# Performance work log

Measured on AMD Instinct MI355X. Metric: run time of the kernel, lower is better.

The kernel has to match this reference:

```python
import jax, jax.numpy as jnp
import numpy as np

EMBED_DIM = 768
NUM_HEADS = 8
HEAD_DIM = EMBED_DIM // NUM_HEADS  # 96
SCALE = HEAD_DIM ** -0.5


def setup_inputs() -> dict:
    key = jax.random.key(0)
    k1, k2, k3 = jax.random.split(key, 3)
    x = jax.random.normal(k1, (2, 4096, EMBED_DIM), dtype=jnp.float32)
    # nn.Linear weights stored [out, in]; init scaled like kaiming-uniform-ish
    w_qkv = jax.random.normal(k2, (3 * EMBED_DIM, EMBED_DIM), dtype=jnp.float32) * (EMBED_DIM ** -0.5)
    w_proj = jax.random.normal(k3, (EMBED_DIM, EMBED_DIM), dtype=jnp.float32) * (EMBED_DIM ** -0.5)
    return {"x": x, "w_qkv": w_qkv, "w_proj": w_proj}


def reference(x, w_qkv, w_proj):
    B, N, C = x.shape
    H, D = NUM_HEADS, C // NUM_HEADS
    qkv = jnp.einsum('bnc,oc->bno', x, w_qkv)          # [B,N,3C]
    qkv = qkv.reshape(B, N, 3, H, D).transpose(2, 0, 3, 1, 4)  # [3,B,H,N,D]
    q, k, v = qkv[0], qkv[1], qkv[2]
    attn = jnp.einsum('bhnd,bhmd->bhnm', q, k) * SCALE  # [B,H,N,N]
    attn = jax.nn.softmax(attn, axis=-1)
    out = jnp.einsum('bhnm,bhmd->bhnd', attn, v)        # [B,H,N,D]
    out = out.transpose(0, 2, 1, 3).reshape(B, N, C)
    out = jnp.einsum('bnc,oc->bno', out, w_proj)        # proj (no bias)
    return out  # dropout p=0.0 -> identity
```

## Files before the change

### kernel.cpp

```cpp
#include <hip/hip_runtime.h>

typedef __bf16 bf16;
typedef __attribute__((ext_vector_type(8))) __bf16 bf16x8;
typedef __attribute__((ext_vector_type(2))) __bf16 bf16x2;
typedef __attribute__((ext_vector_type(4))) float f32x4;
typedef __attribute__((ext_vector_type(16))) float f32x16;
typedef __attribute__((ext_vector_type(8))) unsigned short ushort8;
typedef __attribute__((ext_vector_type(4))) unsigned short ushort4v;

__device__ __forceinline__ unsigned short f2bf(float f) {
    union { float f; unsigned int u; } v; v.f = f;
    unsigned int u = v.u;
    return (unsigned short)((u + 0x7fffu + ((u >> 16) & 1u)) >> 16);
}

#if __has_builtin(__builtin_amdgcn_cvt_pk_bf16_f32)
__device__ __forceinline__ unsigned int pk2bf(float a, float b) {
    union { bf16x2 v; unsigned int u; } c;
    c.v = __builtin_amdgcn_cvt_pk_bf16_f32(a, b);
    return c.u;
}
#else
__device__ __forceinline__ unsigned int pk2bf(float a, float b) {
    return (unsigned int)f2bf(a) | ((unsigned int)f2bf(b) << 16);
}
#endif

__device__ __forceinline__ f32x4 mfma16(bf16x8 a, bf16x8 b, f32x4 c) {
    return __builtin_amdgcn_mfma_f32_16x16x32_bf16(a, b, c, 0, 0, 0);
}
__device__ __forceinline__ f32x16 mfma32(bf16x8 a, bf16x8 b, f32x16 c) {
    return __builtin_amdgcn_mfma_f32_32x32x16_bf16(a, b, c, 0, 0, 0);
}

#if __has_builtin(__builtin_amdgcn_global_load_lds)
__device__ __forceinline__ void gload16(const unsigned short* g, unsigned short* l) {
    typedef const unsigned int __attribute__((address_space(1)))* gp_t;
    typedef unsigned int __attribute__((address_space(3)))* lp_t;
    __builtin_amdgcn_global_load_lds((gp_t)(const void*)g, (lp_t)(void*)l, 16, 0, 0);
}
#define GLL_LANE 1
#else
#define GLL_LANE 0
#endif

__global__ void cvt3_f32_bf16(const float* __restrict__ x, const float* __restrict__ wq,
                              const float* __restrict__ wp,
                              unsigned short* __restrict__ xb, unsigned short* __restrict__ wqb,
                              unsigned short* __restrict__ wpb) {
    int i = blockIdx.x * 256 + threadIdx.x;
    const float* in; unsigned short* out; int base;
    if (i < 1572864)      { in = x;  out = xb;  base = i; }
    else if (i < 2015232) { in = wq; out = wqb; base = i - 1572864; }
    else if (i < 2162688) { in = wp; out = wpb; base = i - 2015232; }
    else return;
    float4 f = reinterpret_cast<const float4*>(in)[base];
    union { ushort4v v; unsigned int u[2]; } o;
    o.u[0] = pk2bf(f.x, f.y);
    o.u[1] = pk2bf(f.z, f.w);
    reinterpret_cast<ushort4v*>(out)[base] = o.v;
}

__device__ __forceinline__ int kperm(int k5) {
    return (k5 & 3) | (((k5 >> 3) & 1) << 2) | (((k5 >> 4) & 1) << 3) | (((k5 >> 2) & 1) << 4);
}
__device__ __forceinline__ int kperm_inv(int p5) {
    return (p5 & 3) | (((p5 >> 4) & 1) << 2) | (((p5 >> 2) & 1) << 3) | (((p5 >> 3) & 1) << 4);
}

__global__ __launch_bounds__(256) void qkv_gemm(const unsigned short* __restrict__ A,
                                                const unsigned short* __restrict__ W,
                                                unsigned short* __restrict__ Qf,
                                                unsigned short* __restrict__ Kf,
                                                unsigned short* __restrict__ Vf) {
    __shared__ __align__(16) char smem[34816];
    unsigned short* As = (unsigned short*)smem;
    unsigned short* Bs = (unsigned short*)(smem + 8192);
    unsigned short* T  = (unsigned short*)smem;
    const int t = threadIdx.x;
    const int w = t >> 6, l = t & 63;
    const int wm = (w >> 1) * 64, wn = (w & 1) * 64;
    const int lr = l & 15, lq = l >> 4;
    const int m0 = blockIdx.y * 128, n0 = blockIdx.x * 128;
    f32x4 acc[4][4] = {};
    for (int k0 = 0; k0 < 768; k0 += 32) {
        __syncthreads();
#pragma unroll
        for (int i = 0; i < 2; ++i) {
            int v = t + i * 256;
            int r = v >> 2, c8 = (v & 3) * 8;
#if GLL_LANE
            gload16(&A[(m0 + r) * 768 + k0 + c8], &As[(w * 64 + i * 256) * 8]);
            gload16(&W[(n0 + r) * 768 + k0 + c8], &Bs[(w * 64 + i * 256) * 8]);
#else
            *reinterpret_cast<ushort8*>(&As[r * 32 + c8]) =
                *reinterpret_cast<const ushort8*>(&A[(m0 + r) * 768 + k0 + c8]);
            *reinterpret_cast<ushort8*>(&Bs[r * 32 + c8]) =
                *reinterpret_cast<const ushort8*>(&W[(n0 + r) * 768 + k0 + c8]);
#endif
        }
        __syncthreads();
        bf16x8 af[4], bfr[4];
#pragma unroll
        for (int mt = 0; mt < 4; ++mt)
            af[mt] = *reinterpret_cast<const bf16x8*>(&As[(wm + mt * 16 + lr) * 32 + lq * 8]);
#pragma unroll
        for (int nt = 0; nt < 4; ++nt)
            bfr[nt] = *reinterpret_cast<const bf16x8*>(&Bs[(wn + nt * 16 + lr) * 32 + lq * 8]);
#pragma unroll
        for (int mt = 0; mt < 4; ++mt)
#pragma unroll
            for (int nt = 0; nt < 4; ++nt)
                acc[mt][nt] = mfma16(af[mt], bfr[nt], acc[mt][nt]);
    }
    const int tsel = n0 / 768;
    __syncthreads();
    if (tsel < 2) {
#pragma unroll
        for (int nt = 0; nt < 4; ++nt)
#pragma unroll
            for (int mt = 0; mt < 4; ++mt)
#pragma unroll
                for (int r = 0; r < 4; ++r) {
                    int row = wm + mt * 16 + lq * 4 + r;
                    int col = wn + nt * 16 + lr;
                    float val = acc[mt][nt][r];
                    if (tsel == 0) val *= 0.14724444f;
                    T[row * 136 + col] = f2bf(val);
                }
    } else {
#pragma unroll
        for (int nt = 0; nt < 4; ++nt)
#pragma unroll
            for (int mt = 0; mt < 4; ++mt)
#pragma unroll
                for (int r = 0; r < 4; ++r) {
                    int row = wm + mt * 16 + lq * 4 + r;
                    int col = wn + nt * 16 + lr;
                    T[col * 136 + row] = f2bf(acc[mt][nt][r]);
                }
    }
    __syncthreads();
    if (tsel < 2) {
#pragma unroll
        for (int i = 0; i < 8; ++i) {
            int idx = t + i * 256;
            int pos31 = idx & 31;
            int rest = idx >> 5;
            int c8 = rest & 15, qg = rest >> 4;
            int l31 = (tsel == 1) ? kperm_inv(pos31) : pos31;
            int gncol = n0 + c8 * 8;
            int rem = gncol - tsel * 768;
            int head = rem / 96, d = rem - head * 96;
            int kq = d >> 4, h2 = (d >> 3) & 1;
            int gm = m0 + qg * 32 + l31;
            int b = gm >> 12, nn = gm & 4095;
            int bh = b * 8 + head;
            long chunk = (long)(bh * 128 + (nn >> 5)) * 6 + kq;
            ushort8 v8 = *reinterpret_cast<const ushort8*>(&T[(qg * 32 + l31) * 136 + c8 * 8]);
            unsigned short* dst = (tsel == 0) ? Qf : Kf;
            *reinterpret_cast<ushort8*>(&dst[(chunk << 9) + ((h2 * 32 + pos31) << 3)]) = v8;
        }
    } else {
#pragma unroll
        for (int i = 0; i < 8; ++i) {
            int idx = t + i * 256;
            int dl = idx & 31;
            int rr = idx >> 5;
            int r8 = rr & 15, cmb = rr >> 4;
            int col = cmb * 32 + dl;
            int gncol = n0 + col;
            int rem = gncol - 1536;
            int head = rem / 96, d = rem - head * 96;
            int dn = d >> 5;
            int keybase = m0 + r8 * 8;
            int b = keybase >> 12, nn = keybase & 4095;
            int kg = nn >> 5, f = (nn >> 4) & 1, hv = (nn >> 3) & 1;
            int bh = b * 8 + head;
            long chunk = (long)(bh * 128 + kg) * 6 + dn * 2 + f;
            ushort8 v8 = *reinterpret_cast<const ushort8*>(&T[col * 136 + r8 * 8]);
            *reinterpret_cast<ushort8*>(&Vf[(chunk << 9) + ((hv * 32 + dl) << 3)]) = v8;
        }
    }
}

__global__ __launch_bounds__(256, 2) void attn_kernel(const unsigned short* __restrict__ Qf,
                                                      const unsigned short* __restrict__ Kf,
                                                      const unsigned short* __restrict__ Vf,
                                                      unsigned short* __restrict__ Og) {
    __shared__ __align__(16) float red[4608];
    const int t = threadIdx.x;
    const int w = t >> 6, l = t & 63;
    const int wr = w >> 1, wk = w & 1;
    const int l31 = l & 31, h = l >> 5;
    const int b0 = blockIdx.x;
    const int kk = b0 >> 3;
    const int bh = (b0 & 7) * 2 + (kk >> 5);
    const int q0 = (kk & 31) * 128;
    const int voff = l << 3;

    bf16x8 aq[2][6];
#pragma unroll
    for (int qn = 0; qn < 2; ++qn) {
        long qb = ((long)((bh * 128 + (q0 >> 5) + wr * 2 + qn) * 6)) << 9;
#pragma unroll
        for (int kq = 0; kq < 6; ++kq)
            aq[qn][kq] = *reinterpret_cast<const bf16x8*>(&Qf[qb + (kq << 9) + voff]);
    }

    f32x16 acc[2][3] = {};
    float lsum0 = 0.f, lsum1 = 0.f;

    for (int it = 0; it < 64; ++it) {
        const int kt = wk * 64 + it;
        const long kbase = ((long)((bh * 128 + kt) * 6)) << 9;
        f32x16 s[2] = {};
#pragma unroll
        for (int kq = 0; kq < 6; ++kq) {
            bf16x8 bk = *reinterpret_cast<const bf16x8*>(&Kf[kbase + (kq << 9) + voff]);
            s[0] = mfma32(bk, aq[0][kq], s[0]);
            s[1] = mfma32(bk, aq[1][kq], s[1]);
        }
        union PF { unsigned int u[4]; bf16x8 v8; } p[2][2];
#pragma unroll
        for (int qn = 0; qn < 2; ++qn) {
            float e[16];
#pragma unroll
            for (int r = 0; r < 16; ++r) e[r] = __builtin_amdgcn_exp2f(s[qn][r]);
            float s0 = (e[0] + e[1]) + (e[2] + e[3]);
            float s1 = (e[4] + e[5]) + (e[6] + e[7]);
            float s2 = (e[8] + e[9]) + (e[10] + e[11]);
            float s3 = (e[12] + e[13]) + (e[14] + e[15]);
            if (qn == 0) lsum0 += (s0 + s1) + (s2 + s3);
            else         lsum1 += (s0 + s1) + (s2 + s3);
#pragma unroll
            for (int f = 0; f < 2; ++f) {
                p[qn][f].u[0] = pk2bf(e[4 * f + 0], e[4 * f + 1]);
                p[qn][f].u[1] = pk2bf(e[4 * f + 2], e[4 * f + 3]);
                p[qn][f].u[2] = pk2bf(e[8 + 4 * f + 0], e[8 + 4 * f + 1]);
                p[qn][f].u[3] = pk2bf(e[8 + 4 * f + 2], e[8 + 4 * f + 3]);
            }
        }
#pragma unroll
        for (int dn = 0; dn < 3; ++dn) {
#pragma unroll
            for (int f = 0; f < 2; ++f) {
                bf16x8 vb = *reinterpret_cast<const bf16x8*>(
                    &Vf[kbase + ((dn * 2 + f) << 9) + voff]);
                acc[0][dn] = mfma32(p[0][f].v8, vb, acc[0][dn]);
                acc[1][dn] = mfma32(p[1][f].v8, vb, acc[1][dn]);
            }
        }
    }

    const int rbase = (wr * 64 + l) * 36;
#pragma unroll
    for (int ps = 0; ps < 3; ++ps) {
        __syncthreads();
        if (wk == 1) {
#pragma unroll
            for (int c = 0; c < 2; ++c) {
                int c2 = ps * 2 + c, qn = c2 / 3, dn = c2 % 3;
#pragma unroll
                for (int u = 0; u < 4; ++u) {
                    f32x4 tmp;
#pragma unroll
                    for (int j = 0; j < 4; ++j) tmp[j] = acc[qn][dn][u * 4 + j];
                    *reinterpret_cast<f32x4*>(&red[rbase + c * 16 + u * 4]) = tmp;
                }
            }
        }
        __syncthreads();
        if (wk == 0) {
#pragma unroll
            for (int c = 0; c < 2; ++c) {
                int c2 = ps * 2 + c, qn = c2 / 3, dn = c2 % 3;
#pragma unroll
                for (int u = 0; u < 4; ++u) {
                    f32x4 tmp = *reinterpret_cast<const f32x4*>(&red[rbase + c * 16 + u * 4]);
#pragma unroll
                    for (int j = 0; j < 4; ++j) acc[qn][dn][u * 4 + j] += tmp[j];
                }
            }
        }
    }

    lsum0 += __shfl_xor(lsum0, 32);
    lsum1 += __shfl_xor(lsum1, 32);
    __syncthreads();
    if (wk == 1 && h == 0) {
        red[(wr * 2 + 0) * 32 + l31] = lsum0;
        red[(wr * 2 + 1) * 32 + l31] = lsum1;
    }
    __syncthreads();
    if (wk == 0 && h == 0) {
        red[128 + (wr * 2 + 0) * 32 + l31] = 1.f / (lsum0 + red[(wr * 2 + 0) * 32 + l31]);
        red[128 + (wr * 2 + 1) * 32 + l31] = 1.f / (lsum1 + red[(wr * 2 + 1) * 32 + l31]);
    }
    __syncthreads();
    if (wk == 0) {
        const int b = bh >> 3, head = bh & 7;
#pragma unroll
        for (int qn = 0; qn < 2; ++qn) {
#pragma unroll
            for (int reg = 0; reg < 16; ++reg) {
                int qloc = (reg & 3) + 8 * (reg >> 2) + 4 * h;
                int n = q0 + wr * 64 + qn * 32 + qloc;
                float inv = red[128 + (wr * 2 + qn) * 32 + qloc];
                int rowoff = (b * 4096 + n) * 768 + head * 96;
#pragma unroll
                for (int dn = 0; dn < 3; ++dn)
                    Og[rowoff + dn * 32 + l31] = f2bf(acc[qn][dn][reg] * inv);
            }
        }
    }
}

__global__ __launch_bounds__(256) void proj_gemm(const unsigned short* __restrict__ A,
                                                 const unsigned short* __restrict__ W,
                                                 float* __restrict__ out) {
    __shared__ __align__(16) unsigned short As[128 * 32];
    __shared__ __align__(16) unsigned short Bs[128 * 32];
    const int t = threadIdx.x;
    const int w = t >> 6, l = t & 63;
    const int wm = (w >> 1) * 64, wn = (w & 1) * 64;
    const int lr = l & 15, lq = l >> 4;
    const int m0 = blockIdx.y * 128, n0 = blockIdx.x * 128;
    f32x4 acc[4][4] = {};
    for (int k0 = 0; k0 < 768; k0 += 32) {
        __syncthreads();
#pragma unroll
        for (int i = 0; i < 2; ++i) {
            int v = t + i * 256;
            int r = v >> 2, c8 = (v & 3) * 8;
#if GLL_LANE
            gload16(&A[(m0 + r) * 768 + k0 + c8], &As[(w * 64 + i * 256) * 8]);
            gload16(&W[(n0 + r) * 768 + k0 + c8], &Bs[(w * 64 + i * 256) * 8]);
#else
            *reinterpret_cast<ushort8*>(&As[r * 32 + c8]) =
                *reinterpret_cast<const ushort8*>(&A[(m0 + r) * 768 + k0 + c8]);
            *reinterpret_cast<ushort8*>(&Bs[r * 32 + c8]) =
                *reinterpret_cast<const ushort8*>(&W[(n0 + r) * 768 + k0 + c8]);
#endif
        }
        __syncthreads();
        bf16x8 af[4], bfr[4];
#pragma unroll
        for (int mt = 0; mt < 4; ++mt)
            af[mt] = *reinterpret_cast<const bf16x8*>(&As[(wm + mt * 16 + lr) * 32 + lq * 8]);
#pragma unroll
        for (int nt = 0; nt < 4; ++nt)
            bfr[nt] = *reinterpret_cast<const bf16x8*>(&Bs[(wn + nt * 16 + lr) * 32 + lq * 8]);
#pragma unroll
        for (int mt = 0; mt < 4; ++mt)
#pragma unroll
            for (int nt = 0; nt < 4; ++nt)
                acc[mt][nt] = mfma16(af[mt], bfr[nt], acc[mt][nt]);
    }
#pragma unroll
    for (int nt = 0; nt < 4; ++nt) {
        int gn = n0 + wn + nt * 16 + lr;
#pragma unroll
        for (int mt = 0; mt < 4; ++mt) {
#pragma unroll
            for (int r = 0; r < 4; ++r) {
                int gm = m0 + wm + mt * 16 + lq * 4 + r;
                out[gm * 768 + gn] = acc[mt][nt][r];
            }
        }
    }
}

extern "C" void kernel_launch(void* const* d_in, const int* in_sizes, int n_in,
                              void* d_out, int out_size, void* d_ws, size_t ws_size,
                              hipStream_t stream) {
    const float* x     = (const float*)d_in[0];
    const float* wqkv  = (const float*)d_in[1];
    const float* wproj = (const float*)d_in[2];
    float* out = (float*)d_out;
    char* ws = (char*)d_ws;
    unsigned short* xb     = (unsigned short*)(ws);
    unsigned short* wqkvb  = (unsigned short*)(ws + 12582912);
    unsigned short* wprojb = (unsigned short*)(ws + 16121856);
    unsigned short* Qf     = (unsigned short*)(ws + 17301504);
    unsigned short* Kf     = (unsigned short*)(ws + 29884416);
    unsigned short* Vf     = (unsigned short*)(ws + 42467328);
    unsigned short* attnb  = xb;

    cvt3_f32_bf16<<<8448, 256, 0, stream>>>(x, wqkv, wproj, xb, wqkvb, wprojb);
    qkv_gemm<<<dim3(18, 64), 256, 0, stream>>>(xb, wqkvb, Qf, Kf, Vf);
    attn_kernel<<<512, 256, 0, stream>>>(Qf, Kf, Vf, attnb);
    proj_gemm<<<dim3(6, 64), 256, 0, stream>>>(attnb, wprojb, out);
}
```

Measured before the change: 270.3 us.

## Halve attention query tile per block to double grid and occupancy

The attention kernel now gives each block 64 query rows instead of 128, so each wave handles one 32-row query slab rather than two. Register and shared-memory use per block roughly halve, launch bounds rise to 4 blocks per CU, and the grid doubles to 1024 blocks, aiming for better latency hiding and CU fill on a 256-CU part. In exchange, each K/V fragment loaded from global memory now feeds only one query slab, doubling K/V traffic per unit of work and lowering MFMA reuse per load.

```diff
diff --git a/kernel.cpp b/kernel.cpp
--- a/kernel.cpp
+++ b/kernel.cpp
@@ -184,62 +184,51 @@
     }
 }
 
-__global__ __launch_bounds__(256, 2) void attn_kernel(const unsigned short* __restrict__ Qf,
+__global__ __launch_bounds__(256, 4) void attn_kernel(const unsigned short* __restrict__ Qf,
                                                       const unsigned short* __restrict__ Kf,
                                                       const unsigned short* __restrict__ Vf,
                                                       unsigned short* __restrict__ Og) {
-    __shared__ __align__(16) float red[4608];
+    __shared__ __align__(16) float red[2560];
     const int t = threadIdx.x;
     const int w = t >> 6, l = t & 63;
     const int wr = w >> 1, wk = w & 1;
     const int l31 = l & 31, h = l >> 5;
     const int b0 = blockIdx.x;
     const int kk = b0 >> 3;
-    const int bh = (b0 & 7) * 2 + (kk >> 5);
-    const int q0 = (kk & 31) * 128;
+    const int bh = (b0 & 7) * 2 + (kk >> 6);
+    const int q0 = (kk & 63) * 64;
     const int voff = l << 3;
 
-    bf16x8 aq[2][6];
-#pragma unroll
-    for (int qn = 0; qn < 2; ++qn) {
-        long qb = ((long)((bh * 128 + (q0 >> 5) + wr * 2 + qn) * 6)) << 9;
+    bf16x8 aq[6];
+    {
+        long qb = ((long)((bh * 128 + (q0 >> 5) + wr) * 6)) << 9;
 #pragma unroll
         for (int kq = 0; kq < 6; ++kq)
-            aq[qn][kq] = *reinterpret_cast<const bf16x8*>(&Qf[qb + (kq << 9) + voff]);
-    }
-
-    f32x16 acc[2][3] = {};
-    float lsum0 = 0.f, lsum1 = 0.f;
+            aq[kq] = *reinterpret_cast<const bf16x8*>(&Qf[qb + (kq << 9) + voff]);
+    }
+
+    f32x16 acc[3] = {};
+    float lsum = 0.f;
 
     for (int it = 0; it < 64; ++it) {
         const int kt = wk * 64 + it;
         const long kbase = ((long)((bh * 128 + kt) * 6)) << 9;
-        f32x16 s[2] = {};
+        f32x16 s = {};
 #pragma unroll
         for (int kq = 0; kq < 6; ++kq) {
             bf16x8 bk = *reinterpret_cast<const bf16x8*>(&Kf[kbase + (kq << 9) + voff]);
-            s[0] = mfma32(bk, aq[0][kq], s[0]);
-            s[1] = mfma32(bk, aq[1][kq], s[1]);
-        }
-        union PF { unsigned int u[4]; bf16x8 v8; } p[2][2];
-#pragma unroll
-        for (int qn = 0; qn < 2; ++qn) {
-            float e[16];
-#pragma unroll
-            for (int r = 0; r < 16; ++r) e[r] = __builtin_amdgcn_exp2f(s[qn][r]);
-            float s0 = (e[0] + e[1]) + (e[2] + e[3]);
-            float s1 = (e[4] + e[5]) + (e[6] + e[7]);
-            float s2 = (e[8] + e[9]) + (e[10] + e[11]);
-            float s3 = (e[12] + e[13]) + (e[14] + e[15]);
-            if (qn == 0) lsum0 += (s0 + s1) + (s2 + s3);
-            else         lsum1 += (s0 + s1) + (s2 + s3);
-#pragma unroll
-            for (int f = 0; f < 2; ++f) {
-                p[qn][f].u[0] = pk2bf(e[4 * f + 0], e[4 * f + 1]);
-                p[qn][f].u[1] = pk2bf(e[4 * f + 2], e[4 * f + 3]);
-                p[qn][f].u[2] = pk2bf(e[8 + 4 * f + 0], e[8 + 4 * f + 1]);
-                p[qn][f].u[3] = pk2bf(e[8 + 4 * f + 2], e[8 + 4 * f + 3]);
-            }
+            s = mfma32(bk, aq[kq], s);
+        }
+        union PF { unsigned int u[4]; bf16x8 v8; } p[2];
+#pragma unroll
+        for (int g = 0; g < 4; ++g) {
+            float e0 = __builtin_amdgcn_exp2f(s[4 * g + 0]);
+            float e1 = __builtin_amdgcn_exp2f(s[4 * g + 1]);
+            float e2 = __builtin_amdgcn_exp2f(s[4 * g + 2]);
+            float e3 = __builtin_amdgcn_exp2f(s[4 * g + 3]);
+            lsum += (e0 + e1) + (e2 + e3);
+            p[g & 1].u[(g >> 1) * 2 + 0] = pk2bf(e0, e1);
+            p[g & 1].u[(g >> 1) * 2 + 1] = pk2bf(e2, e3);
         }
 #pragma unroll
         for (int dn = 0; dn < 3; ++dn) {
@@ -247,71 +236,53 @@
             for (int f = 0; f < 2; ++f) {
                 bf16x8 vb = *reinterpret_cast<const bf16x8*>(
                     &Vf[kbase + ((dn * 2 + f) << 9) + voff]);
-                acc[0][dn] = mfma32(p[0][f].v8, vb, acc[0][dn]);
-                acc[1][dn] = mfma32(p[1][f].v8, vb, acc[1][dn]);
+                acc[dn] = mfma32(p[f].v8, vb, acc[dn]);
             }
         }
     }
 
-    const int rbase = (wr * 64 + l) * 36;
+    const int rbase = (wr * 64 + l) * 20;
 #pragma unroll
     for (int ps = 0; ps < 3; ++ps) {
         __syncthreads();
         if (wk == 1) {
 #pragma unroll
-            for (int c = 0; c < 2; ++c) {
-                int c2 = ps * 2 + c, qn = c2 / 3, dn = c2 % 3;
-#pragma unroll
-                for (int u = 0; u < 4; ++u) {
-                    f32x4 tmp;
-#pragma unroll
-                    for (int j = 0; j < 4; ++j) tmp[j] = acc[qn][dn][u * 4 + j];
-                    *reinterpret_cast<f32x4*>(&red[rbase + c * 16 + u * 4]) = tmp;
-                }
+            for (int u = 0; u < 4; ++u) {
+                f32x4 tmp;
+#pragma unroll
+                for (int j = 0; j < 4; ++j) tmp[j] = acc[ps][u * 4 + j];
+                *reinterpret_cast<f32x4*>(&red[rbase + u * 4]) = tmp;
             }
         }
         __syncthreads();
         if (wk == 0) {
 #pragma unroll
-            for (int c = 0; c < 2; ++c) {
-                int c2 = ps * 2 + c, qn = c2 / 3, dn = c2 % 3;
-#pragma unroll
-                for (int u = 0; u < 4; ++u) {
-                    f32x4 tmp = *reinterpret_cast<const f32x4*>(&red[rbase + c * 16 + u * 4]);
-#pragma unroll
-                    for (int j = 0; j < 4; ++j) acc[qn][dn][u * 4 + j] += tmp[j];
-                }
+            for (int u = 0; u < 4; ++u) {
+                f32x4 tmp = *reinterpret_cast<const f32x4*>(&red[rbase + u * 4]);
+#pragma unroll
+                for (int j = 0; j < 4; ++j) acc[ps][u * 4 + j] += tmp[j];
             }
         }
     }
 
-    lsum0 += __shfl_xor(lsum0, 32);
-    lsum1 += __shfl_xor(lsum1, 32);
-    __syncthreads();
-    if (wk == 1 && h == 0) {
-        red[(wr * 2 + 0) * 32 + l31] = lsum0;
-        red[(wr * 2 + 1) * 32 + l31] = lsum1;
-    }
-    __syncthreads();
-    if (wk == 0 && h == 0) {
-        red[128 + (wr * 2 + 0) * 32 + l31] = 1.f / (lsum0 + red[(wr * 2 + 0) * 32 + l31]);
-        red[128 + (wr * 2 + 1) * 32 + l31] = 1.f / (lsum1 + red[(wr * 2 + 1) * 32 + l31]);
-    }
+    lsum += __shfl_xor(lsum, 32);
+    __syncthreads();
+    if (wk == 1 && h == 0) red[wr * 32 + l31] = lsum;
+    __syncthreads();
+    if (wk == 0 && h == 0)
+        red[64 + wr * 32 + l31] = 1.f / (lsum + red[wr * 32 + l31]);
     __syncthreads();
     if (wk == 0) {
         const int b = bh >> 3, head = bh & 7;
 #pragma unroll
-        for (int qn = 0; qn < 2; ++qn) {
-#pragma unroll
-            for (int reg = 0; reg < 16; ++reg) {
-                int qloc = (reg & 3) + 8 * (reg >> 2) + 4 * h;
-                int n = q0 + wr * 64 + qn * 32 + qloc;
-                float inv = red[128 + (wr * 2 + qn) * 32 + qloc];
-                int rowoff = (b * 4096 + n) * 768 + head * 96;
-#pragma unroll
-                for (int dn = 0; dn < 3; ++dn)
-                    Og[rowoff + dn * 32 + l31] = f2bf(acc[qn][dn][reg] * inv);
-            }
+        for (int reg = 0; reg < 16; ++reg) {
+            int qloc = (reg & 3) + 8 * (reg >> 2) + 4 * h;
+            int n = q0 + wr * 32 + qloc;
+            float inv = red[64 + wr * 32 + qloc];
+            int rowoff = (b * 4096 + n) * 768 + head * 96;
+#pragma unroll
+            for (int dn = 0; dn < 3; ++dn)
+                Og[rowoff + dn * 32 + l31] = f2bf(acc[dn][reg] * inv);
         }
     }
 }
@@ -389,6 +360,6 @@
 
     cvt3_f32_bf16<<<8448, 256, 0, stream>>>(x, wqkv, wproj, xb, wqkvb, wprojb);
     qkv_gemm<<<dim3(18, 64), 256, 0, stream>>>(xb, wqkvb, Qf, Kf, Vf);
-    attn_kernel<<<512, 256, 0, stream>>>(Qf, Kf, Vf, attnb);
+    attn_kernel<<<1024, 256, 0, stream>>>(Qf, Kf, Vf, attnb);
     proj_gemm<<<dim3(6, 64), 256, 0, stream>>>(attnb, wprojb, out);
 }
```

After: 288.8 us. 6.8% more time.

## Double GEMM K-step to 64 and interleave softmax exp with PV MFMAs

Applied to the files above, without the earlier changes.

The QKV and projection GEMMs now load a 64-wide K slab per iteration, as two 32-wide sub-tiles in one shared buffer, which halves the number of barrier pairs per tile. In the attention loop the exponentials are computed in two halves, each followed right away by its PV MFMAs, so transcendental work can overlap matrix-core work and fewer bf16 P registers are live at once. The cost is twice the shared memory per GEMM block, which may reduce occupancy.

```diff
diff --git a/kernel.cpp b/kernel.cpp
--- a/kernel.cpp
+++ b/kernel.cpp
@@ -75,7 +75,6 @@
                                                 unsigned short* __restrict__ Vf) {
     __shared__ __align__(16) char smem[34816];
     unsigned short* As = (unsigned short*)smem;
-    unsigned short* Bs = (unsigned short*)(smem + 8192);
     unsigned short* T  = (unsigned short*)smem;
     const int t = threadIdx.x;
     const int w = t >> 6, l = t & 63;
@@ -83,20 +82,26 @@
     const int lr = l & 15, lq = l >> 4;
     const int m0 = blockIdx.y * 128, n0 = blockIdx.x * 128;
     f32x4 acc[4][4] = {};
-    for (int k0 = 0; k0 < 768; k0 += 32) {
-        __syncthreads();
-#pragma unroll
-        for (int i = 0; i < 2; ++i) {
+    for (int k0 = 0; k0 < 768; k0 += 64) {
+        __syncthreads();
+#pragma unroll
+        for (int i = 0; i < 4; ++i) {
             int v = t + i * 256;
-            int r = v >> 2, c8 = (v & 3) * 8;
+            int sub = v >> 9;
+            int vin = v & 511;
+            int r = vin >> 2, c8 = (vin & 3) * 8;
+            int gcol = k0 + sub * 32 + c8;
 #if GLL_LANE
-            gload16(&A[(m0 + r) * 768 + k0 + c8], &As[(w * 64 + i * 256) * 8]);
-            gload16(&W[(n0 + r) * 768 + k0 + c8], &Bs[(w * 64 + i * 256) * 8]);
+            int vbase = w * 64 + i * 256;
+            int subu = vbase >> 9;
+            unsigned short* dA = &As[subu * 4096 + (vbase & 511) * 8];
+            gload16(&A[(m0 + r) * 768 + gcol], dA);
+            gload16(&W[(n0 + r) * 768 + gcol], dA + 8192);
 #else
-            *reinterpret_cast<ushort8*>(&As[r * 32 + c8]) =
-                *reinterpret_cast<const ushort8*>(&A[(m0 + r) * 768 + k0 + c8]);
-            *reinterpret_cast<ushort8*>(&Bs[r * 32 + c8]) =
-                *reinterpret_cast<const ushort8*>(&W[(n0 + r) * 768 + k0 + c8]);
+            *reinterpret_cast<ushort8*>(&As[sub * 4096 + vin * 8]) =
+                *reinterpret_cast<const ushort8*>(&A[(m0 + r) * 768 + gcol]);
+            *reinterpret_cast<ushort8*>(&As[8192 + sub * 4096 + vin * 8]) =
+                *reinterpret_cast<const ushort8*>(&W[(n0 + r) * 768 + gcol]);
 #endif
         }
         __syncthreads();
@@ -106,7 +111,18 @@
             af[mt] = *reinterpret_cast<const bf16x8*>(&As[(wm + mt * 16 + lr) * 32 + lq * 8]);
 #pragma unroll
         for (int nt = 0; nt < 4; ++nt)
-            bfr[nt] = *reinterpret_cast<const bf16x8*>(&Bs[(wn + nt * 16 + lr) * 32 + lq * 8]);
+            bfr[nt] = *reinterpret_cast<const bf16x8*>(&As[8192 + (wn + nt * 16 + lr) * 32 + lq * 8]);
+#pragma unroll
+        for (int mt = 0; mt < 4; ++mt)
+#pragma unroll
+            for (int nt = 0; nt < 4; ++nt)
+                acc[mt][nt] = mfma16(af[mt], bfr[nt], acc[mt][nt]);
+#pragma unroll
+        for (int mt = 0; mt < 4; ++mt)
+            af[mt] = *reinterpret_cast<const bf16x8*>(&As[4096 + (wm + mt * 16 + lr) * 32 + lq * 8]);
+#pragma unroll
+        for (int nt = 0; nt < 4; ++nt)
+            bfr[nt] = *reinterpret_cast<const bf16x8*>(&As[12288 + (wn + nt * 16 + lr) * 32 + lq * 8]);
 #pragma unroll
         for (int mt = 0; mt < 4; ++mt)
 #pragma unroll
@@ -221,35 +237,50 @@
             s[0] = mfma32(bk, aq[0][kq], s[0]);
             s[1] = mfma32(bk, aq[1][kq], s[1]);
         }
-        union PF { unsigned int u[4]; bf16x8 v8; } p[2][2];
+        union PF { unsigned int u[4]; bf16x8 v8; } p0[2], p1[2];
 #pragma unroll
         for (int qn = 0; qn < 2; ++qn) {
-            float e[16];
-#pragma unroll
-            for (int r = 0; r < 16; ++r) e[r] = __builtin_amdgcn_exp2f(s[qn][r]);
-            float s0 = (e[0] + e[1]) + (e[2] + e[3]);
-            float s1 = (e[4] + e[5]) + (e[6] + e[7]);
-            float s2 = (e[8] + e[9]) + (e[10] + e[11]);
-            float s3 = (e[12] + e[13]) + (e[14] + e[15]);
-            if (qn == 0) lsum0 += (s0 + s1) + (s2 + s3);
-            else         lsum1 += (s0 + s1) + (s2 + s3);
-#pragma unroll
-            for (int f = 0; f < 2; ++f) {
-                p[qn][f].u[0] = pk2bf(e[4 * f + 0], e[4 * f + 1]);
-                p[qn][f].u[1] = pk2bf(e[4 * f + 2], e[4 * f + 3]);
-                p[qn][f].u[2] = pk2bf(e[8 + 4 * f + 0], e[8 + 4 * f + 1]);
-                p[qn][f].u[3] = pk2bf(e[8 + 4 * f + 2], e[8 + 4 * f + 3]);
-            }
+            float ea = __builtin_amdgcn_exp2f(s[qn][0]);
+            float eb = __builtin_amdgcn_exp2f(s[qn][1]);
+            float ec = __builtin_amdgcn_exp2f(s[qn][2]);
+            float ed = __builtin_amdgcn_exp2f(s[qn][3]);
+            float ee = __builtin_amdgcn_exp2f(s[qn][8]);
+            float ef = __builtin_amdgcn_exp2f(s[qn][9]);
+            float eg = __builtin_amdgcn_exp2f(s[qn][10]);
+            float eh = __builtin_amdgcn_exp2f(s[qn][11]);
+            float part = ((ea + eb) + (ec + ed)) + ((ee + ef) + (eg + eh));
+            if (qn == 0) lsum0 += part; else lsum1 += part;
+            p0[qn].u[0] = pk2bf(ea, eb); p0[qn].u[1] = pk2bf(ec, ed);
+            p0[qn].u[2] = pk2bf(ee, ef); p0[qn].u[3] = pk2bf(eg, eh);
         }
 #pragma unroll
         for (int dn = 0; dn < 3; ++dn) {
-#pragma unroll
-            for (int f = 0; f < 2; ++f) {
-                bf16x8 vb = *reinterpret_cast<const bf16x8*>(
-                    &Vf[kbase + ((dn * 2 + f) << 9) + voff]);
-                acc[0][dn] = mfma32(p[0][f].v8, vb, acc[0][dn]);
-                acc[1][dn] = mfma32(p[1][f].v8, vb, acc[1][dn]);
-            }
+            bf16x8 vb = *reinterpret_cast<const bf16x8*>(
+                &Vf[kbase + ((dn * 2) << 9) + voff]);
+            acc[0][dn] = mfma32(p0[0].v8, vb, acc[0][dn]);
+            acc[1][dn] = mfma32(p0[1].v8, vb, acc[1][dn]);
+        }
+#pragma unroll
+        for (int qn = 0; qn < 2; ++qn) {
+            float ea = __builtin_amdgcn_exp2f(s[qn][4]);
+            float eb = __builtin_amdgcn_exp2f(s[qn][5]);
+            float ec = __builtin_amdgcn_exp2f(s[qn][6]);
+            float ed = __builtin_amdgcn_exp2f(s[qn][7]);
+            float ee = __builtin_amdgcn_exp2f(s[qn][12]);
+            float ef = __builtin_amdgcn_exp2f(s[qn][13]);
+            float eg = __builtin_amdgcn_exp2f(s[qn][14]);
+            float eh = __builtin_amdgcn_exp2f(s[qn][15]);
+            float part = ((ea + eb) + (ec + ed)) + ((ee + ef) + (eg + eh));
+            if (qn == 0) lsum0 += part; else lsum1 += part;
+            p1[qn].u[0] = pk2bf(ea, eb); p1[qn].u[1] = pk2bf(ec, ed);
+            p1[qn].u[2] = pk2bf(ee, ef); p1[qn].u[3] = pk2bf(eg, eh);
+        }
+#pragma unroll
+        for (int dn = 0; dn < 3; ++dn) {
+            bf16x8 vb = *reinterpret_cast<const bf16x8*>(
+                &Vf[kbase + ((dn * 2 + 1) << 9) + voff]);
+            acc[0][dn] = mfma32(p1[0].v8, vb, acc[0][dn]);
+            acc[1][dn] = mfma32(p1[1].v8, vb, acc[1][dn]);
         }
     }
 
@@ -319,28 +350,33 @@
 __global__ __launch_bounds__(256) void proj_gemm(const unsigned short* __restrict__ A,
                                                  const unsigned short* __restrict__ W,
                                                  float* __restrict__ out) {
-    __shared__ __align__(16) unsigned short As[128 * 32];
-    __shared__ __align__(16) unsigned short Bs[128 * 32];
+    __shared__ __align__(16) unsigned short As[16384];
     const int t = threadIdx.x;
     const int w = t >> 6, l = t & 63;
     const int wm = (w >> 1) * 64, wn = (w & 1) * 64;
     const int lr = l & 15, lq = l >> 4;
     const int m0 = blockIdx.y * 128, n0 = blockIdx.x * 128;
     f32x4 acc[4][4] = {};
-    for (int k0 = 0; k0 < 768; k0 += 32) {
-        __syncthreads();
-#pragma unroll
-        for (int i = 0; i < 2; ++i) {
+    for (int k0 = 0; k0 < 768; k0 += 64) {
+        __syncthreads();
+#pragma unroll
+        for (int i = 0; i < 4; ++i) {
             int v = t + i * 256;
-            int r = v >> 2, c8 = (v & 3) * 8;
+            int sub = v >> 9;
+            int vin = v & 511;
+            int r = vin >> 2, c8 = (vin & 3) * 8;
+            int gcol = k0 + sub * 32 + c8;
 #if GLL_LANE
-            gload16(&A[(m0 + r) * 768 + k0 + c8], &As[(w * 64 + i * 256) * 8]);
-            gload16(&W[(n0 + r) * 768 + k0 + c8], &Bs[(w * 64 + i * 256) * 8]);
+            int vbase = w * 64 + i * 256;
+            int subu = vbase >> 9;
+            unsigned short* dA = &As[subu * 4096 + (vbase & 511) * 8];
+            gload16(&A[(m0 + r) * 768 + gcol], dA);
+            gload16(&W[(n0 + r) * 768 + gcol], dA + 8192);
 #else
-            *reinterpret_cast<ushort8*>(&As[r * 32 + c8]) =
-                *reinterpret_cast<const ushort8*>(&A[(m0 + r) * 768 + k0 + c8]);
-            *reinterpret_cast<ushort8*>(&Bs[r * 32 + c8]) =
-                *reinterpret_cast<const ushort8*>(&W[(n0 + r) * 768 + k0 + c8]);
+            *reinterpret_cast<ushort8*>(&As[sub * 4096 + vin * 8]) =
+                *reinterpret_cast<const ushort8*>(&A[(m0 + r) * 768 + gcol]);
+            *reinterpret_cast<ushort8*>(&As[8192 + sub * 4096 + vin * 8]) =
+                *reinterpret_cast<const ushort8*>(&W[(n0 + r) * 768 + gcol]);
 #endif
         }
         __syncthreads();
@@ -350,7 +386,18 @@
             af[mt] = *reinterpret_cast<const bf16x8*>(&As[(wm + mt * 16 + lr) * 32 + lq * 8]);
 #pragma unroll
         for (int nt = 0; nt < 4; ++nt)
-            bfr[nt] = *reinterpret_cast<const bf16x8*>(&Bs[(wn + nt * 16 + lr) * 32 + lq * 8]);
+            bfr[nt] = *reinterpret_cast<const bf16x8*>(&As[8192 + (wn + nt * 16 + lr) * 32 + lq * 8]);
+#pragma unroll
+        for (int mt = 0; mt < 4; ++mt)
+#pragma unroll
+            for (int nt = 0; nt < 4; ++nt)
+                acc[mt][nt] = mfma16(af[mt], bfr[nt], acc[mt][nt]);
+#pragma unroll
+        for (int mt = 0; mt < 4; ++mt)
+            af[mt] = *reinterpret_cast<const bf16x8*>(&As[4096 + (wm + mt * 16 + lr) * 32 + lq * 8]);
+#pragma unroll
+        for (int nt = 0; nt < 4; ++nt)
+            bfr[nt] = *reinterpret_cast<const bf16x8*>(&As[12288 + (wn + nt * 16 + lr) * 32 + lq * 8]);
 #pragma unroll
         for (int mt = 0; mt < 4; ++mt)
 #pragma unroll
```

New measurement: 269.2 us. No clear change (-0.4%).

## Double-buffer LDS tiles in QKV and projection GEMMs

Applied to the files above, without the earlier changes.

Both the QKV and output-projection GEMMs now use two LDS buffers. The next K-slice is loaded into the idle buffer while MFMAs consume the current one, which cuts one barrier per iteration and overlaps global loads with compute. LDS use per block doubles for proj_gemm. The attention kernel, which likely dominates runtime, is untouched, so the overall effect is limited to the GEMM share.

```diff
diff --git a/kernel.cpp b/kernel.cpp
--- a/kernel.cpp
+++ b/kernel.cpp
@@ -74,47 +74,65 @@
                                                 unsigned short* __restrict__ Kf,
                                                 unsigned short* __restrict__ Vf) {
     __shared__ __align__(16) char smem[34816];
-    unsigned short* As = (unsigned short*)smem;
-    unsigned short* Bs = (unsigned short*)(smem + 8192);
-    unsigned short* T  = (unsigned short*)smem;
+    unsigned short* S = (unsigned short*)smem;
+    unsigned short* T = (unsigned short*)smem;
     const int t = threadIdx.x;
     const int w = t >> 6, l = t & 63;
     const int wm = (w >> 1) * 64, wn = (w & 1) * 64;
     const int lr = l & 15, lq = l >> 4;
     const int m0 = blockIdx.y * 128, n0 = blockIdx.x * 128;
     f32x4 acc[4][4] = {};
-    for (int k0 = 0; k0 < 768; k0 += 32) {
-        __syncthreads();
-#pragma unroll
-        for (int i = 0; i < 2; ++i) {
-            int v = t + i * 256;
-            int r = v >> 2, c8 = (v & 3) * 8;
+
 #if GLL_LANE
-            gload16(&A[(m0 + r) * 768 + k0 + c8], &As[(w * 64 + i * 256) * 8]);
-            gload16(&W[(n0 + r) * 768 + k0 + c8], &Bs[(w * 64 + i * 256) * 8]);
+#define QSTAGE(ks, boff)                                                        \
+    {                                                                           \
+        const int k0s = (ks) * 32;                                              \
+        _Pragma("unroll")                                                       \
+        for (int i = 0; i < 2; ++i) {                                           \
+            int v = t + i * 256;                                                \
+            int r = v >> 2, c8 = (v & 3) * 8;                                   \
+            unsigned short* dst = &S[(boff) + (w * 64 + i * 256) * 8];          \
+            gload16(&A[(m0 + r) * 768 + k0s + c8], dst);                        \
+            gload16(&W[(n0 + r) * 768 + k0s + c8], dst + 4096);                 \
+        }                                                                       \
+    }
 #else
-            *reinterpret_cast<ushort8*>(&As[r * 32 + c8]) =
-                *reinterpret_cast<const ushort8*>(&A[(m0 + r) * 768 + k0 + c8]);
-            *reinterpret_cast<ushort8*>(&Bs[r * 32 + c8]) =
-                *reinterpret_cast<const ushort8*>(&W[(n0 + r) * 768 + k0 + c8]);
+#define QSTAGE(ks, boff)                                                        \
+    {                                                                           \
+        const int k0s = (ks) * 32;                                              \
+        _Pragma("unroll")                                                       \
+        for (int i = 0; i < 2; ++i) {                                           \
+            int v = t + i * 256;                                                \
+            int r = v >> 2, c8 = (v & 3) * 8;                                   \
+            *reinterpret_cast<ushort8*>(&S[(boff) + v * 8]) =                   \
+                *reinterpret_cast<const ushort8*>(&A[(m0 + r) * 768 + k0s + c8]);\
+            *reinterpret_cast<ushort8*>(&S[(boff) + 4096 + v * 8]) =            \
+                *reinterpret_cast<const ushort8*>(&W[(n0 + r) * 768 + k0s + c8]);\
+        }                                                                       \
+    }
 #endif
-        }
-        __syncthreads();
+
+    QSTAGE(0, 0);
+    __syncthreads();
+    for (int ks = 0; ks < 24; ++ks) {
+        const int cur = (ks & 1) ? 8192 : 0;
+        if (ks < 23) QSTAGE(ks + 1, 8192 - cur);
         bf16x8 af[4], bfr[4];
 #pragma unroll
         for (int mt = 0; mt < 4; ++mt)
-            af[mt] = *reinterpret_cast<const bf16x8*>(&As[(wm + mt * 16 + lr) * 32 + lq * 8]);
+            af[mt] = *reinterpret_cast<const bf16x8*>(&S[cur + (wm + mt * 16 + lr) * 32 + lq * 8]);
 #pragma unroll
         for (int nt = 0; nt < 4; ++nt)
-            bfr[nt] = *reinterpret_cast<const bf16x8*>(&Bs[(wn + nt * 16 + lr) * 32 + lq * 8]);
+            bfr[nt] = *reinterpret_cast<const bf16x8*>(&S[cur + 4096 + (wn + nt * 16 + lr) * 32 + lq * 8]);
 #pragma unroll
         for (int mt = 0; mt < 4; ++mt)
 #pragma unroll
             for (int nt = 0; nt < 4; ++nt)
                 acc[mt][nt] = mfma16(af[mt], bfr[nt], acc[mt][nt]);
-    }
+        __syncthreads();
+    }
+#undef QSTAGE
     const int tsel = n0 / 768;
-    __syncthreads();
     if (tsel < 2) {
 #pragma unroll
         for (int nt = 0; nt < 4; ++nt)
@@ -319,44 +337,63 @@
 __global__ __launch_bounds__(256) void proj_gemm(const unsigned short* __restrict__ A,
                                                  const unsigned short* __restrict__ W,
                                                  float* __restrict__ out) {
-    __shared__ __align__(16) unsigned short As[128 * 32];
-    __shared__ __align__(16) unsigned short Bs[128 * 32];
+    __shared__ __align__(16) unsigned short S[16384];
     const int t = threadIdx.x;
     const int w = t >> 6, l = t & 63;
     const int wm = (w >> 1) * 64, wn = (w & 1) * 64;
     const int lr = l & 15, lq = l >> 4;
     const int m0 = blockIdx.y * 128, n0 = blockIdx.x * 128;
     f32x4 acc[4][4] = {};
-    for (int k0 = 0; k0 < 768; k0 += 32) {
-        __syncthreads();
-#pragma unroll
-        for (int i = 0; i < 2; ++i) {
-            int v = t + i * 256;
-            int r = v >> 2, c8 = (v & 3) * 8;
+
 #if GLL_LANE
-            gload16(&A[(m0 + r) * 768 + k0 + c8], &As[(w * 64 + i * 256) * 8]);
-            gload16(&W[(n0 + r) * 768 + k0 + c8], &Bs[(w * 64 + i * 256) * 8]);
+#define PSTAGE(ks, boff)                                                        \
+    {                                                                           \
+        const int k0s = (ks) * 32;                                              \
+        _Pragma("unroll")                                                       \
+        for (int i = 0; i < 2; ++i) {                                           \
+            int v = t + i * 256;                                                \
+            int r = v >> 2, c8 = (v & 3) * 8;                                   \
+            unsigned short* dst = &S[(boff) + (w * 64 + i * 256) * 8];          \
+            gload16(&A[(m0 + r) * 768 + k0s + c8], dst);                        \
+            gload16(&W[(n0 + r) * 768 + k0s + c8], dst + 4096);                 \
+        }                                                                       \
+    }
 #else
-            *reinterpret_cast<ushort8*>(&As[r * 32 + c8]) =
-                *reinterpret_cast<const ushort8*>(&A[(m0 + r) * 768 + k0 + c8]);
-            *reinterpret_cast<ushort8*>(&Bs[r * 32 + c8]) =
-                *reinterpret_cast<const ushort8*>(&W[(n0 + r) * 768 + k0 + c8]);
+#define PSTAGE(ks, boff)                                                        \
+    {                                                                           \
+        const int k0s = (ks) * 32;                                              \
+        _Pragma("unroll")                                                       \
+        for (int i = 0; i < 2; ++i) {                                           \
+            int v = t + i * 256;                                                \
+            int r = v >> 2, c8 = (v & 3) * 8;                                   \
+            *reinterpret_cast<ushort8*>(&S[(boff) + v * 8]) =                   \
+                *reinterpret_cast<const ushort8*>(&A[(m0 + r) * 768 + k0s + c8]);\
+            *reinterpret_cast<ushort8*>(&S[(boff) + 4096 + v * 8]) =            \
+                *reinterpret_cast<const ushort8*>(&W[(n0 + r) * 768 + k0s + c8]);\
+        }                                                                       \
+    }
 #endif
-        }
-        __syncthreads();
+
+    PSTAGE(0, 0);
+    __syncthreads();
+    for (int ks = 0; ks < 24; ++ks) {
+        const int cur = (ks & 1) ? 8192 : 0;
+        if (ks < 23) PSTAGE(ks + 1, 8192 - cur);
         bf16x8 af[4], bfr[4];
 #pragma unroll
         for (int mt = 0; mt < 4; ++mt)
-            af[mt] = *reinterpret_cast<const bf16x8*>(&As[(wm + mt * 16 + lr) * 32 + lq * 8]);
+            af[mt] = *reinterpret_cast<const bf16x8*>(&S[cur + (wm + mt * 16 + lr) * 32 + lq * 8]);
 #pragma unroll
         for (int nt = 0; nt < 4; ++nt)
-            bfr[nt] = *reinterpret_cast<const bf16x8*>(&Bs[(wn + nt * 16 + lr) * 32 + lq * 8]);
+            bfr[nt] = *reinterpret_cast<const bf16x8*>(&S[cur + 4096 + (wn + nt * 16 + lr) * 32 + lq * 8]);
 #pragma unroll
         for (int mt = 0; mt < 4; ++mt)
 #pragma unroll
             for (int nt = 0; nt < 4; ++nt)
                 acc[mt][nt] = mfma16(af[mt], bfr[nt], acc[mt][nt]);
-    }
+        __syncthreads();
+    }
+#undef PSTAGE
 #pragma unroll
     for (int nt = 0; nt < 4; ++nt) {
         int gn = n0 + wn + nt * 16 + lr;
```

Result: faster. 262.0 us (-3.1%).
